# Optimization experiments

Measured on AMD Instinct MI355X. Metric: run time of the kernel, lower is better.

Reference implementation:

```python
import jax, jax.numpy as jnp
import numpy as np

N, E, D = 50000, 800000, 128
NODE_IN, EDGE_IN, STEPS = 19, 4, 5
EPS = 1e-5

def leaky(x):
    return jnp.where(x > 0, x, 0.05 * x)

def mlp3(x, W1, b1, W2, b2, W3, b3):
    x = leaky(x @ W1 + b1)
    x = leaky(x @ W2 + b2)
    return x @ W3 + b3

def layer_norm(x, g, b):
    m = jnp.mean(x, axis=-1, keepdims=True)
    v = jnp.var(x, axis=-1, keepdims=True)
    return (x - m) * jax.lax.rsqrt(v + EPS) * g + b

def batch_norm(x, g, b):
    # training-mode BatchNorm1d: biased batch stats over node dim
    m = jnp.mean(x, axis=0)
    v = jnp.var(x, axis=0)
    return (x - m) * jax.lax.rsqrt(v + EPS) * g + b

def gcn_conv(x, src, dst, W, b):
    # PyG GCNConv: add self loops, sym-normalize by deg^{-1/2}, aggregate at dst
    h = x @ W  # [N, D]
    deg = jax.ops.segment_sum(jnp.ones(E, x.dtype), dst, num_segments=N) + 1.0
    dis = jax.lax.rsqrt(deg)
    msg = h[src] * (dis[src] * dis[dst])[:, None]  # [E, D]
    agg = jax.ops.segment_sum(msg, dst, num_segments=N) + h * (dis * dis)[:, None]
    return agg + b


def setup_inputs() -> dict:
    key = jax.random.key(0)
    ks = iter(jax.random.split(key, 64))
    w = lambda shape: jax.random.normal(next(ks), shape, jnp.float32) * 0.05
    z = lambda: jnp.zeros((D,), jnp.float32)
    o = lambda: jnp.ones((D,), jnp.float32)
    inp = {
        'node_feat': jax.random.normal(next(ks), (N, NODE_IN), jnp.float32),
        'edge_feat': jax.random.normal(next(ks), (E, EDGE_IN), jnp.float32),
        'edge_index': jax.random.randint(next(ks), (2, E), 0, N, jnp.int32),
        'enc_node_W1': w((NODE_IN, D)), 'enc_node_b1': z(),
        'enc_node_W2': w((D, D)), 'enc_node_b2': z(),
        'enc_node_W3': w((D, D)), 'enc_node_b3': z(),
        'enc_node_ln_g': o(), 'enc_node_ln_b': z(),
        'enc_edge_W1': w((EDGE_IN, D)), 'enc_edge_b1': z(),
        'enc_edge_W2': w((D, D)), 'enc_edge_b2': z(),
        'enc_edge_W3': w((D, D)), 'enc_edge_b3': z(),
        'enc_edge_ln_g': o(), 'enc_edge_ln_b': z(),
        'proc_W': w((STEPS, 2, D, D)),
        'proc_b': jnp.zeros((STEPS, 2, D), jnp.float32),
        'proc_bn_g': jnp.ones((STEPS, D), jnp.float32),
        'proc_bn_b': jnp.zeros((STEPS, D), jnp.float32),
        'dec_W1': w((D, D)), 'dec_b1': z(),
        'dec_W2': w((D, D)), 'dec_b2': z(),
        'dec_W3': w((D, D)), 'dec_b3': z(),
        'dec_ln_g': o(), 'dec_ln_b': z(),
    }
    return inp


def reference(node_feat, edge_feat, edge_index,
              enc_node_W1, enc_node_b1, enc_node_W2, enc_node_b2, enc_node_W3, enc_node_b3,
              enc_node_ln_g, enc_node_ln_b,
              enc_edge_W1, enc_edge_b1, enc_edge_W2, enc_edge_b2, enc_edge_W3, enc_edge_b3,
              enc_edge_ln_g, enc_edge_ln_b,
              proc_W, proc_b, proc_bn_g, proc_bn_b,
              dec_W1, dec_b1, dec_W2, dec_b2, dec_W3, dec_b3, dec_ln_g, dec_ln_b):
    src, dst = edge_index[0], edge_index[1]
    # encode
    hn = layer_norm(mlp3(node_feat, enc_node_W1, enc_node_b1, enc_node_W2, enc_node_b2,
                         enc_node_W3, enc_node_b3), enc_node_ln_g, enc_node_ln_b)
    he = layer_norm(mlp3(edge_feat, enc_edge_W1, enc_edge_b1, enc_edge_W2, enc_edge_b2,
                         enc_edge_W3, enc_edge_b3), enc_edge_ln_g, enc_edge_ln_b)
    # scatter-mean edge features onto source nodes
    cnt = jax.ops.segment_sum(jnp.ones(E, hn.dtype), src, num_segments=N)
    hn = hn + jax.ops.segment_sum(he, src, num_segments=N) / jnp.maximum(cnt, 1.0)[:, None]
    # 5 residual GCN processor steps (GCNConv -> LeakyReLU -> BN -> GCNConv)
    for s in range(STEPS):
        x = gcn_conv(hn, src, dst, proc_W[s, 0], proc_b[s, 0])
        x = batch_norm(leaky(x), proc_bn_g[s], proc_bn_b[s])
        x = gcn_conv(x, src, dst, proc_W[s, 1], proc_b[s, 1])
        hn = hn + x
    # decode
    return layer_norm(mlp3(hn, dec_W1, dec_b1, dec_W2, dec_b2, dec_W3, dec_b3),
                      dec_ln_g, dec_ln_b)
```

## Files before the change

### kernel.cpp

```cpp
#include <hip/hip_runtime.h>

#define NN 50000
#define NE 800000
#define DD 128
#define LN_EPS 1e-5f

typedef __attribute__((ext_vector_type(8))) short v8s;
typedef __attribute__((ext_vector_type(4))) unsigned v4u;
typedef __attribute__((ext_vector_type(4))) float f32x4;
typedef __attribute__((ext_vector_type(2))) float f32x2;

union CvtHL { v4u u; v8s s; };

__device__ __forceinline__ float leakyf(float x){ return x > 0.f ? x : 0.05f*x; }
__device__ __forceinline__ short f2bf(float f){
  unsigned u = __float_as_uint(f);
  u = (u + 0x7fffu + ((u >> 16) & 1u)) >> 16;
  return (short)u;
}
__device__ __forceinline__ float bf2f(unsigned short h){
  return __uint_as_float(((unsigned)h) << 16);
}
__device__ __forceinline__ unsigned cvt_pk_bf16(float a, float b){
  unsigned r;
  asm("v_cvt_pk_bf16_f32 %0, %1, %2" : "=v"(r) : "v"(a), "v"(b));
  return r;
}
__device__ __forceinline__ f32x2 pk_add(f32x2 a, f32x2 b){
  f32x2 r; asm("v_pk_add_f32 %0, %1, %2" : "=v"(r) : "v"(a), "v"(b)); return r;
}
__device__ __forceinline__ f32x2 pk_mul(f32x2 a, f32x2 b){
  f32x2 r; asm("v_pk_mul_f32 %0, %1, %2" : "=v"(r) : "v"(a), "v"(b)); return r;
}
__device__ __forceinline__ unsigned pack_hi16(unsigned u0, unsigned u1){
  return __builtin_amdgcn_perm(u1, u0, 0x07060302u);
}
__device__ __forceinline__ short2 f2bf2v(float v){
  unsigned u = __float_as_uint(v);
  short hi = (short)(u >> 16);
  float lo = v - __uint_as_float(u & 0xffff0000u);
  return make_short2(hi, f2bf(lo));
}

__global__ void pack_w_kernel(const float* __restrict__ W, short* __restrict__ Wh,
                              short* __restrict__ Wl, int K, int Kp)
{
  int idx = blockIdx.x*256 + threadIdx.x;
  if (idx >= Kp*128) return;
  int k = idx >> 7, n = idx & 127;
  float v = (k < K) ? W[k*128 + n] : 0.f;
  short2 t = f2bf2v(v);
  size_t o = ((size_t)(k >> 3)*128 + n)*8 + (k & 7);
  Wh[o] = t.x; Wl[o] = t.y;
}

__global__ void pack_edge_w1_kernel(const float* __restrict__ W1, const float* __restrict__ b1,
                                    short* __restrict__ Wp)
{
  int idx = blockIdx.x*256 + threadIdx.x;
  if (idx >= 32*128) return;
  int k = idx >> 7, n = idx & 127;
  short v = 0;
  if (k < 4)        v = f2bf2v(W1[k*128 + n]).x;
  else if (k < 8)   v = f2bf2v(W1[(k-4)*128 + n]).y;
  else if (k < 12)  v = f2bf2v(W1[(k-8)*128 + n]).x;
  else if (k == 12) v = f2bf2v(b1[n]).x;
  else if (k == 13) v = f2bf2v(b1[n]).y;
  size_t o = ((size_t)(k >> 3)*128 + n)*8 + (k & 7);
  Wp[o] = v;
}

#define NPACK 11
struct PackArgs { const float* src[NPACK]; short* dh[NPACK]; short* dl[NPACK]; };

__global__ void pack_many_kernel(PackArgs pa)
{
  int m = blockIdx.y;
  int idx = blockIdx.x*256 + threadIdx.x;
  int k = idx >> 7, n = idx & 127;
  float v = pa.src[m][k*128 + n];
  short2 t = f2bf2v(v);
  size_t o = ((size_t)(k >> 3)*128 + n)*8 + (k & 7);
  pa.dh[m][o] = t.x; pa.dl[m][o] = t.y;
}

#define MFMA3(ah, al, bh, bl, ac) \
  ac = __builtin_amdgcn_mfma_f32_16x16x32_bf16(al, bh, ac, 0,0,0); \
  ac = __builtin_amdgcn_mfma_f32_16x16x32_bf16(ah, bl, ac, 0,0,0); \
  ac = __builtin_amdgcn_mfma_f32_16x16x32_bf16(ah, bh, ac, 0,0,0);

#define MFMA2(ah, bh, bl, ac) \
  ac = __builtin_amdgcn_mfma_f32_16x16x32_bf16(ah, bl, ac, 0,0,0); \
  ac = __builtin_amdgcn_mfma_f32_16x16x32_bf16(ah, bh, ac, 0,0,0);

#define SPLIT8(f0, f1, h, l) { \
  unsigned u0=__float_as_uint(f0.x), u1=__float_as_uint(f0.y), u2=__float_as_uint(f0.z), u3=__float_as_uint(f0.w); \
  unsigned u4=__float_as_uint(f1.x), u5=__float_as_uint(f1.y), u6=__float_as_uint(f1.z), u7=__float_as_uint(f1.w); \
  CvtHL ch_, cl_; \
  ch_.u = (v4u){ pack_hi16(u0,u1), pack_hi16(u2,u3), pack_hi16(u4,u5), pack_hi16(u6,u7) }; \
  cl_.u = (v4u){ \
    cvt_pk_bf16(f0.x-__uint_as_float(u0&0xffff0000u), f0.y-__uint_as_float(u1&0xffff0000u)), \
    cvt_pk_bf16(f0.z-__uint_as_float(u2&0xffff0000u), f0.w-__uint_as_float(u3&0xffff0000u)), \
    cvt_pk_bf16(f1.x-__uint_as_float(u4&0xffff0000u), f1.y-__uint_as_float(u5&0xffff0000u)), \
    cvt_pk_bf16(f1.z-__uint_as_float(u6&0xffff0000u), f1.w-__uint_as_float(u7&0xffff0000u)) }; \
  h = ch_.s; l = cl_.s; }

#define EPI_PK(accv, bv2, DOBIAS, p01, p23) { \
  f32x2 x01 = (f32x2){(accv)[0], (accv)[1]}; \
  f32x2 x23 = (f32x2){(accv)[2], (accv)[3]}; \
  if (DOBIAS) { x01 = pk_add(x01, bv2); x23 = pk_add(x23, bv2); } \
  f32x2 m01 = pk_mul(x01, (f32x2)(0.05f)); \
  f32x2 m23 = pk_mul(x23, (f32x2)(0.05f)); \
  p01 = cvt_pk_bf16(fmaxf(x01.x, m01.x), fmaxf(x01.y, m01.y)); \
  p23 = cvt_pk_bf16(fmaxf(x23.x, m23.x), fmaxf(x23.y, m23.y)); }

template<int IN_W, bool SCATTER>
__global__ __launch_bounds__(256)
void mlp_mfma_kernel(const float* __restrict__ x, int nrows,
                     const short* __restrict__ W1h, const short* __restrict__ W1l,
                     const float* __restrict__ b1,
                     const short* __restrict__ W2h, const short* __restrict__ W2l,
                     const float* __restrict__ b2,
                     const short* __restrict__ W3h, const short* __restrict__ W3l,
                     const float* __restrict__ b3,
                     const float* __restrict__ g, const float* __restrict__ bb,
                     float* __restrict__ out,
                     const int* __restrict__ sidx,
                     const int* __restrict__ eperm)
{
  constexpr int L1K = (IN_W + 31) / 32;
  constexpr bool EDGE1 = (SCATTER && IN_W == 4);
  __shared__ __align__(16) short Hh[128*136];
  __shared__ float lnS[128][2], lnQ[128][2];
  __shared__ int sidx_s[128];
  __shared__ __align__(16) uint4 xstage[SCATTER ? 128 : 1];

  const int tid  = threadIdx.x;
  const int lane = tid & 63, wave = tid >> 6;
  const int wr = wave >> 1, wc = wave & 1;
  const int quad = lane >> 4, low = lane & 15;
  const int row0 = blockIdx.x * 128;

  if (SCATTER) {
    if (tid < 128) {
      int e = eperm[row0 + tid];
      float4 f = ((const float4*)x)[e];
      unsigned u0=__float_as_uint(f.x), u1=__float_as_uint(f.y);
      unsigned u2=__float_as_uint(f.z), u3=__float_as_uint(f.w);
      uint4 st;
      st.x = pack_hi16(u0,u1);
      st.y = pack_hi16(u2,u3);
      st.z = cvt_pk_bf16(f.x-__uint_as_float(u0&0xffff0000u), f.y-__uint_as_float(u1&0xffff0000u));
      st.w = cvt_pk_bf16(f.z-__uint_as_float(u2&0xffff0000u), f.w-__uint_as_float(u3&0xffff0000u));
      xstage[tid] = st;
      sidx_s[tid] = sidx[row0 + tid];
    }
    __syncthreads();
  }

  f32x4 acc[4][4];

  #pragma unroll
  for (int tm=0;tm<4;tm++)
    #pragma unroll
    for (int tn=0;tn<4;tn++) acc[tm][tn] = (f32x4)0.f;

  if constexpr (EDGE1) {
    v8s ah[4], bh[4];
    #pragma unroll
    for (int tm=0;tm<4;tm++) {
      int lr = wr*64 + tm*16 + low;
      v8s h = (v8s)0;
      if (quad == 0) {
        uint4 st = xstage[lr];
        CvtHL c_; c_.u = (v4u){ st.x, st.y, st.x, st.y };
        h = c_.s;
      } else if (quad == 1) {
        uint4 st = xstage[lr];
        CvtHL c_; c_.u = (v4u){ st.z, st.w, 0x3F803F80u, 0u };
        h = c_.s;
      }
      ah[tm] = h;
    }
    #pragma unroll
    for (int tn=0;tn<4;tn++) {
      size_t o = ((size_t)quad*128 + wc*64 + tn*16 + low)*8;
      bh[tn] = *(const v8s*)(W1h + o);
    }
    #pragma unroll
    for (int tm=0;tm<4;tm++)
      #pragma unroll
      for (int tn=0;tn<4;tn++)
        acc[tm][tn] = __builtin_amdgcn_mfma_f32_16x16x32_bf16(ah[tm], bh[tn], acc[tm][tn], 0,0,0);
  } else {
    for (int ks = 0; ks < L1K; ks++) {
      v8s ah[4], al[4], bh[4], bl[4];
      #pragma unroll
      for (int tm=0;tm<4;tm++) {
        int lr = wr*64 + tm*16 + low;
        v8s h = (v8s)0, l = (v8s)0;
        if (IN_W % 32 == 0) {
          int r = row0 + lr;
          if (r < nrows) {
            const float* p = x + (size_t)r*IN_W + ks*32 + quad*8;
            float4 f0 = *(const float4*)p;
            float4 f1 = *(const float4*)(p + 4);
            SPLIT8(f0, f1, h, l);
          }
        } else {
          int r = row0 + lr;
          #pragma unroll
          for (int j=0;j<8;j++) {
            int k = ks*32 + quad*8 + j;
            if (k < IN_W && r < nrows) {
              short2 t = f2bf2v(x[(size_t)r*IN_W + k]);
              h[j] = t.x; l[j] = t.y;
            }
          }
        }
        ah[tm] = h; al[tm] = l;
      }
      #pragma unroll
      for (int tn=0;tn<4;tn++) {
        size_t o = ((size_t)(ks*4+quad)*128 + wc*64 + tn*16 + low)*8;
        bh[tn] = *(const v8s*)(W1h + o);
        bl[tn] = *(const v8s*)(W1l + o);
      }
      #pragma unroll
      for (int tm=0;tm<4;tm++)
        #pragma unroll
        for (int tn=0;tn<4;tn++) { MFMA3(ah[tm], al[tm], bh[tn], bl[tn], acc[tm][tn]); }
    }
  }
  #pragma unroll
  for (int tn=0;tn<4;tn++) {
    float bv = EDGE1 ? 0.f : b1[wc*64 + tn*16 + low];
    f32x2 bv2 = (f32x2)(bv);
    #pragma unroll
    for (int tm=0;tm<4;tm++) {
      unsigned p01, p23;
      EPI_PK(acc[tm][tn], bv2, !EDGE1, p01, p23);
      int base = (wr*64+tm*16+quad*4)*136 + wc*64+tn*16+low;
      Hh[base]     = (short)p01;
      Hh[base+136] = (short)(p01>>16);
      Hh[base+272] = (short)p23;
      Hh[base+408] = (short)(p23>>16);
    }
  }
  __syncthreads();

  #pragma unroll
  for (int tm=0;tm<4;tm++)
    #pragma unroll
    for (int tn=0;tn<4;tn++) acc[tm][tn] = (f32x4)0.f;
  #pragma unroll
  for (int ks=0;ks<4;ks++) {
    v8s ah[4], bh[4], bl[4];
    #pragma unroll
    for (int tm=0;tm<4;tm++)
      ah[tm] = *(const v8s*)&Hh[(wr*64+tm*16+low)*136 + ks*32 + quad*8];
    #pragma unroll
    for (int tn=0;tn<4;tn++) {
      size_t o = ((size_t)(ks*4+quad)*128 + wc*64 + tn*16 + low)*8;
      bh[tn] = *(const v8s*)(W2h + o);
      bl[tn] = *(const v8s*)(W2l + o);
    }
    #pragma unroll
    for (int tm=0;tm<4;tm++)
      #pragma unroll
      for (int tn=0;tn<4;tn++) { MFMA2(ah[tm], bh[tn], bl[tn], acc[tm][tn]); }
  }
  __syncthreads();
  #pragma unroll
  for (int tn=0;tn<4;tn++) {
    float bv = b2[wc*64 + tn*16 + low];
    f32x2 bv2 = (f32x2)(bv);
    #pragma unroll
    for (int tm=0;tm<4;tm++) {
      unsigned p01, p23;
      EPI_PK(acc[tm][tn], bv2, true, p01, p23);
      int base = (wr*64+tm*16+quad*4)*136 + wc*64+tn*16+low;
      Hh[base]     = (short)p01;
      Hh[base+136] = (short)(p01>>16);
      Hh[base+272] = (short)p23;
      Hh[base+408] = (short)(p23>>16);
    }
  }
  __syncthreads();

  #pragma unroll
  for (int tm=0;tm<4;tm++)
    #pragma unroll
    for (int tn=0;tn<4;tn++) acc[tm][tn] = (f32x4)0.f;
  #pragma unroll
  for (int ks=0;ks<4;ks++) {
    v8s ah[4], bh[4], bl[4];
    #pragma unroll
    for (int tm=0;tm<4;tm++)
      ah[tm] = *(const v8s*)&Hh[(wr*64+tm*16+low)*136 + ks*32 + quad*8];
    #pragma unroll
    for (int tn=0;tn<4;tn++) {
      size_t o = ((size_t)(ks*4+quad)*128 + wc*64 + tn*16 + low)*8;
      bh[tn] = *(const v8s*)(W3h + o);
      bl[tn] = *(const v8s*)(W3l + o);
    }
    #pragma unroll
    for (int tm=0;tm<4;tm++)
      #pragma unroll
      for (int tn=0;tn<4;tn++) { MFMA2(ah[tm], bh[tn], bl[tn], acc[tm][tn]); }
  }
  #pragma unroll
  for (int tn=0;tn<4;tn++) {
    float bv = b3[wc*64 + tn*16 + low];
    #pragma unroll
    for (int tm=0;tm<4;tm++)
      #pragma unroll
      for (int i=0;i<4;i++) acc[tm][tn][i] += bv;
  }

  {
    float ct[16];
    #pragma unroll
    for (int tm=0;tm<4;tm++)
      #pragma unroll
      for (int i=0;i<4;i++)
        ct[tm*4+i] = acc[tm][0][i] + acc[tm][1][i] + acc[tm][2][i] + acc[tm][3][i];
    #pragma unroll
    for (int st=0; st<4; st++) {
      const int mm = 1 << st;
      const bool hbit = ((low >> st) & 1) != 0;
      #pragma unroll
      for (int p=0; p < (16>>st); p+=2) {
        float snd = hbit ? ct[p]   : ct[p+1];
        float kp  = hbit ? ct[p+1] : ct[p];
        ct[p>>1] = kp + __shfl_xor(snd, mm);
      }
    }
    { int r = wr*64 + (low>>2)*16 + quad*4 + (low&3); lnS[r][wc] = ct[0]; }
    #pragma unroll
    for (int tm=0;tm<4;tm++)
      #pragma unroll
      for (int i=0;i<4;i++)
        ct[tm*4+i] = acc[tm][0][i]*acc[tm][0][i] + acc[tm][1][i]*acc[tm][1][i]
                   + acc[tm][2][i]*acc[tm][2][i] + acc[tm][3][i]*acc[tm][3][i];
    #pragma unroll
    for (int st=0; st<4; st++) {
      const int mm = 1 << st;
      const bool hbit = ((low >> st) & 1) != 0;
      #pragma unroll
      for (int p=0; p < (16>>st); p+=2) {
        float snd = hbit ? ct[p]   : ct[p+1];
        float kp  = hbit ? ct[p+1] : ct[p];
        ct[p>>1] = kp + __shfl_xor(snd, mm);
      }
    }
    { int r = wr*64 + (low>>2)*16 + quad*4 + (low&3); lnQ[r][wc] = ct[0]; }
  }
  __syncthreads();

  float g4[4], bb4[4];
  #pragma unroll
  for (int tn=0;tn<4;tn++) { int c = wc*64+tn*16+low; g4[tn] = g[c]; bb4[tn] = bb[c]; }

  #pragma unroll
  for (int tm=0;tm<4;tm++)
    #pragma unroll
    for (int i=0;i<4;i++) {
      int r = wr*64 + tm*16 + quad*4 + i;
      float2 S2 = *(const float2*)&lnS[r][0];
      float2 Q2 = *(const float2*)&lnQ[r][0];
      float s = S2.x + S2.y;
      float q = Q2.x + Q2.y;
      float m = s * (1.f/128.f);
      float var = q * (1.f/128.f) - m*m;
      float rs = rsqrtf(var + LN_EPS);
      int gr = row0 + r;
      if (!SCATTER && gr >= nrows) continue;
      float v0 = (acc[tm][0][i] - m) * rs * g4[0] + bb4[0];
      float v1 = (acc[tm][1][i] - m) * rs * g4[1] + bb4[1];
      float v2 = (acc[tm][2][i] - m) * rs * g4[2] + bb4[2];
      float v3 = (acc[tm][3][i] - m) * rs * g4[3] + bb4[3];
      if (SCATTER) {
        unsigned p01 = cvt_pk_bf16(v0, v1), p23 = cvt_pk_bf16(v2, v3);
        int base = r*132 + wc*64 + low;
        Hh[base]    = (short)p01;
        Hh[base+16] = (short)(p01>>16);
        Hh[base+32] = (short)p23;
        Hh[base+48] = (short)(p23>>16);
      } else {
        size_t ob = (size_t)gr*DD + wc*64 + low;
        out[ob]    = v0;
        out[ob+16] = v1;
        out[ob+32] = v2;
        out[ob+48] = v3;
      }
    }

  if (SCATTER) {
    __syncthreads();
    const unsigned* H32 = (const unsigned*)Hh;
    int cp = tid & 63;
    int gI = tid >> 6;
    int rbeg = gI*32, rend = rbeg + 32;
    unsigned pv = H32[rbeg*66 + cp];
    float a0 = __uint_as_float(pv << 16), a1 = __uint_as_float(pv & 0xffff0000u);
    int cur = sidx_s[rbeg];
    for (int r = rbeg + 1; r < rend; r++) {
      int sv = sidx_s[r];
      unsigned hv = H32[r*66 + cp];
      if (sv != cur) {
        atomicAdd(&out[(size_t)cur*DD + 2*cp],     a0);
        atomicAdd(&out[(size_t)cur*DD + 2*cp + 1], a1);
        a0 = __uint_as_float(hv << 16); a1 = __uint_as_float(hv & 0xffff0000u);
        cur = sv;
      } else {
        a0 += __uint_as_float(hv << 16); a1 += __uint_as_float(hv & 0xffff0000u);
      }
    }
    atomicAdd(&out[(size_t)cur*DD + 2*cp],     a0);
    atomicAdd(&out[(size_t)cur*DD + 2*cp + 1], a1);
  }
}

__global__ __launch_bounds__(256)
void gemm_mfma_kernel(const float* __restrict__ x,
                      const short* __restrict__ Wh, const short* __restrict__ Wl,
                      const float* __restrict__ initv, const float* __restrict__ rowscale,
                      unsigned short* __restrict__ outbf, int nrows)
{
  const int tid  = threadIdx.x;
  const int lane = tid & 63, wave = tid >> 6;
  const int wr = wave >> 1, wc = wave & 1;
  const int quad = lane >> 4, low = lane & 15;
  const int row0 = blockIdx.x * 64;

  f32x4 acc[2][4];
  #pragma unroll
  for (int tm=0;tm<2;tm++)
    #pragma unroll
    for (int tn=0;tn<4;tn++) acc[tm][tn] = (f32x4)0.f;

  #pragma unroll
  for (int ks=0;ks<4;ks++) {
    v8s ah[2], al[2], bh[4], bl[4];
    #pragma unroll
    for (int tm=0;tm<2;tm++) {
      int r = row0 + wr*32 + tm*16 + low;
      v8s h = (v8s)0, l = (v8s)0;
      if (r < nrows) {
        const float* p = x + (size_t)r*DD + ks*32 + quad*8;
        float4 f0 = *(const float4*)p;
        float4 f1 = *(const float4*)(p + 4);
        SPLIT8(f0, f1, h, l);
      }
      ah[tm] = h; al[tm] = l;
    }
    #pragma unroll
    for (int tn=0;tn<4;tn++) {
      size_t o = ((size_t)(ks*4+quad)*128 + wc*64 + tn*16 + low)*8;
      bh[tn] = *(const v8s*)(Wh + o);
      bl[tn] = *(const v8s*)(Wl + o);
    }
    #pragma unroll
    for (int tm=0;tm<2;tm++)
      #pragma unroll
      for (int tn=0;tn<4;tn++) { MFMA3(ah[tm], al[tm], bh[tn], bl[tn], acc[tm][tn]); }
  }

  float iv4[4];
  #pragma unroll
  for (int tn=0;tn<4;tn++) iv4[tn] = initv ? initv[wc*64 + tn*16 + low] : 0.f;

  #pragma unroll
  for (int tm=0;tm<2;tm++)
    #pragma unroll
    for (int i=0;i<4;i++) {
      int gr = row0 + wr*32 + tm*16 + quad*4 + i;
      if (gr >= nrows) continue;
      float sc = rowscale ? rowscale[gr] : 1.f;
      float v0 = (acc[tm][0][i] + iv4[0]) * sc;
      float v1 = (acc[tm][1][i] + iv4[1]) * sc;
      float v2 = (acc[tm][2][i] + iv4[2]) * sc;
      float v3 = (acc[tm][3][i] + iv4[3]) * sc;
      unsigned p01 = cvt_pk_bf16(v0, v1), p23 = cvt_pk_bf16(v2, v3);
      size_t base = (size_t)gr*DD + wc*64 + low;
      outbf[base]    = (unsigned short)p01;
      outbf[base+16] = (unsigned short)(p01>>16);
      outbf[base+32] = (unsigned short)p23;
      outbf[base+48] = (unsigned short)(p23>>16);
    }
}

__global__ __launch_bounds__(256)
void gemm_bf_mfma_kernel(const unsigned short* __restrict__ xb,
                         const short* __restrict__ Wh, const short* __restrict__ Wl,
                         const float* __restrict__ initv, const float* __restrict__ rowscale,
                         unsigned short* __restrict__ outbf, int nrows)
{
  const int tid  = threadIdx.x;
  const int lane = tid & 63, wave = tid >> 6;
  const int wr = wave >> 1, wc = wave & 1;
  const int quad = lane >> 4, low = lane & 15;
  const int row0 = blockIdx.x * 64;

  f32x4 acc[2][4];
  #pragma unroll
  for (int tm=0;tm<2;tm++)
    #pragma unroll
    for (int tn=0;tn<4;tn++) acc[tm][tn] = (f32x4)0.f;

  #pragma unroll
  for (int ks=0;ks<4;ks++) {
    v8s ah[2], bh[4], bl[4];
    #pragma unroll
    for (int tm=0;tm<2;tm++) {
      int r = row0 + wr*32 + tm*16 + low;
      ah[tm] = (r < nrows) ? *(const v8s*)(xb + (size_t)r*DD + ks*32 + quad*8) : (v8s)0;
    }
    #pragma unroll
    for (int tn=0;tn<4;tn++) {
      size_t o = ((size_t)(ks*4+quad)*128 + wc*64 + tn*16 + low)*8;
      bh[tn] = *(const v8s*)(Wh + o);
      bl[tn] = *(const v8s*)(Wl + o);
    }
    #pragma unroll
    for (int tm=0;tm<2;tm++)
      #pragma unroll
      for (int tn=0;tn<4;tn++) { MFMA2(ah[tm], bh[tn], bl[tn], acc[tm][tn]); }
  }

  float iv4[4];
  #pragma unroll
  for (int tn=0;tn<4;tn++) iv4[tn] = initv ? initv[wc*64 + tn*16 + low] : 0.f;

  #pragma unroll
  for (int tm=0;tm<2;tm++)
    #pragma unroll
    for (int i=0;i<4;i++) {
      int gr = row0 + wr*32 + tm*16 + quad*4 + i;
      if (gr >= nrows) continue;
      float sc = rowscale ? rowscale[gr] : 1.f;
      float v0 = (acc[tm][0][i] + iv4[0]) * sc;
      float v1 = (acc[tm][1][i] + iv4[1]) * sc;
      float v2 = (acc[tm][2][i] + iv4[2]) * sc;
      float v3 = (acc[tm][3][i] + iv4[3]) * sc;
      unsigned p01 = cvt_pk_bf16(v0, v1), p23 = cvt_pk_bf16(v2, v3);
      size_t base = (size_t)gr*DD + wc*64 + low;
      outbf[base]    = (unsigned short)p01;
      outbf[base+16] = (unsigned short)(p01>>16);
      outbf[base+32] = (unsigned short)p23;
      outbf[base+48] = (unsigned short)(p23>>16);
    }
}

#define ADD8(a, vv) { \
  a[0] += __uint_as_float((vv).x << 16); a[1] += __uint_as_float((vv).x & 0xffff0000u); \
  a[2] += __uint_as_float((vv).y << 16); a[3] += __uint_as_float((vv).y & 0xffff0000u); \
  a[4] += __uint_as_float((vv).z << 16); a[5] += __uint_as_float((vv).z & 0xffff0000u); \
  a[6] += __uint_as_float((vv).w << 16); a[7] += __uint_as_float((vv).w & 0xffff0000u); }

__global__ __launch_bounds__(256)
void gcn_agg_kernel(const unsigned* __restrict__ hb, const int* __restrict__ rowptr,
                    const int* __restrict__ csr_src, const float* __restrict__ dis,
                    const float* __restrict__ bias, const float* __restrict__ resid,
                    float* __restrict__ outf, unsigned* __restrict__ outb, int mode)
{
  const int wv = __builtin_amdgcn_readfirstlane(threadIdx.x >> 6);
  const int lane = threadIdx.x & 63;
  const int q4 = lane >> 4;
  const int c4 = lane & 15;
  const uint4* hb4 = (const uint4*)hb;
  for (int i = blockIdx.x*4 + wv; i < NN; i += gridDim.x*4) {
    const int beg = rowptr[i], end = rowptr[i+1];
    float a[8];
    #pragma unroll
    for (int t=0;t<8;t++) a[t] = 0.f;
    if (q4 == 0) {
      uint4 sv = hb4[(size_t)i*16 + c4];
      ADD8(a, sv);
    }
    int j = beg;
    for (; j + 16 <= end; j += 16) {
      uint4 v[4];
      #pragma unroll
      for (int k=0;k<4;k++) {
        int s0=csr_src[j+4*k], s1=csr_src[j+4*k+1], s2=csr_src[j+4*k+2], s3=csr_src[j+4*k+3];
        int s = q4==0 ? s0 : q4==1 ? s1 : q4==2 ? s2 : s3;
        v[k] = hb4[(size_t)s*16 + c4];
      }
      #pragma unroll
      for (int k=0;k<4;k++) ADD8(a, v[k]);
    }
    for (; j + 4 <= end; j += 4) {
      int s0=csr_src[j], s1=csr_src[j+1], s2=csr_src[j+2], s3=csr_src[j+3];
      int s = q4==0 ? s0 : q4==1 ? s1 : q4==2 ? s2 : s3;
      uint4 v = hb4[(size_t)s*16 + c4];
      ADD8(a, v);
    }
    if (j < end) {
      int rem = end - j;
      int s = csr_src[j + (q4 < rem ? q4 : 0)];
      uint4 v = hb4[(size_t)s*16 + c4];
      if (q4 < rem) ADD8(a, v);
    }
    #pragma unroll
    for (int t=0;t<8;t++) { a[t] += __shfl_xor(a[t], 16); a[t] += __shfl_xor(a[t], 32); }
    float di = dis[i];
    float4 b0 = ((const float4*)bias)[2*c4], b1 = ((const float4*)bias)[2*c4+1];
    a[0]=a[0]*di+b0.x; a[1]=a[1]*di+b0.y; a[2]=a[2]*di+b0.z; a[3]=a[3]*di+b0.w;
    a[4]=a[4]*di+b1.x; a[5]=a[5]*di+b1.y; a[6]=a[6]*di+b1.z; a[7]=a[7]*di+b1.w;
    if (mode == 0) {
      if (q4 == 0) {
        uint4 pk;
        pk.x = cvt_pk_bf16(leakyf(a[0]), leakyf(a[1]));
        pk.y = cvt_pk_bf16(leakyf(a[2]), leakyf(a[3]));
        pk.z = cvt_pk_bf16(leakyf(a[4]), leakyf(a[5]));
        pk.w = cvt_pk_bf16(leakyf(a[6]), leakyf(a[7]));
        ((uint4*)outb)[(size_t)i*16 + c4] = pk;
      }
    } else {
      if (q4 == 0) {
        float4 r0 = ((const float4*)resid)[(size_t)i*32 + 2*c4];
        float4 r1 = ((const float4*)resid)[(size_t)i*32 + 2*c4+1];
        r0.x+=a[0]; r0.y+=a[1]; r0.z+=a[2]; r0.w+=a[3];
        r1.x+=a[4]; r1.y+=a[5]; r1.z+=a[6]; r1.w+=a[7];
        ((float4*)outf)[(size_t)i*32 + 2*c4]   = r0;
        ((float4*)outf)[(size_t)i*32 + 2*c4+1] = r1;
      }
    }
  }
}

__global__ void count_kernel(const int* __restrict__ src, const int* __restrict__ dst,
                             int* __restrict__ cnt_src, int* __restrict__ deg_dst)
{
  int e = blockIdx.x*blockDim.x + threadIdx.x;
  if (e < NE) {
    atomicAdd(&cnt_src[src[e]], 1);
    atomicAdd(&deg_dst[dst[e]], 1);
  }
}

__global__ void scan2_kernel(const int* __restrict__ a0, int* __restrict__ r0, int* __restrict__ n0,
                             float* __restrict__ aux0,
                             const int* __restrict__ a1, int* __restrict__ r1, int* __restrict__ n1,
                             float* __restrict__ aux1)
{
  const int* a = blockIdx.x ? a1 : a0;
  int* r = blockIdx.x ? r1 : r0;
  int* n = blockIdx.x ? n1 : n0;
  float* aux = blockIdx.x ? aux1 : aux0;
  const int T = 256;
  int tid = threadIdx.x;
  int chunk = (NN + T - 1) / T;
  int begin = tid*chunk, end = begin + chunk; if (end > NN) end = NN; if (begin > NN) begin = NN;
  int s = 0;
  for (int i = begin; i < end; i++) s += a[i];
  __shared__ int ps[T];
  ps[tid] = s; __syncthreads();
  for (int off = 1; off < T; off <<= 1) {
    int v = 0;
    if (tid >= off) v = ps[tid - off];
    __syncthreads();
    if (tid >= off) ps[tid] += v;
    __syncthreads();
  }
  int base = (tid == 0) ? 0 : ps[tid-1];
  for (int i = begin; i < end; i++) {
    r[i] = base; n[i] = base; base += a[i];
    aux[i] = blockIdx.x ? (1.0f / fmaxf((float)a[i], 1.0f)) : rsqrtf((float)a[i] + 1.0f);
  }
  if (tid == T-1) r[NN] = base;
}

__global__ void fill_both_kernel(const int* __restrict__ src, const int* __restrict__ dst,
                                 int* __restrict__ nextp, int* __restrict__ csr_src,
                                 int* __restrict__ nexts, int* __restrict__ eperm,
                                 int* __restrict__ srcsorted)
{
  int e = blockIdx.x*blockDim.x + threadIdx.x;
  if (e < NE) {
    int s = src[e];
    int pos = atomicAdd(&nextp[dst[e]], 1);
    csr_src[pos] = s;
    int ps = atomicAdd(&nexts[s], 1);
    eperm[ps] = e;
    srcsorted[ps] = s;
  }
}

__global__ void addmean_kernel(float* __restrict__ hn, const float* __restrict__ nodesum,
                               const float* __restrict__ invcnt)
{
  int t = blockIdx.x*blockDim.x + threadIdx.x;
  if (t < NN*DD/4) {
    float4 a = ((const float4*)hn)[t];
    float4 b = ((const float4*)nodesum)[t];
    float ic = invcnt[t >> 5];
    a.x += b.x*ic; a.y += b.y*ic; a.z += b.z*ic; a.w += b.w*ic;
    ((float4*)hn)[t] = a;
  }
}

__global__ __launch_bounds__(256)
void bn_stats_kernel(const unsigned short* __restrict__ yb, float* __restrict__ sums)
{
  int col = threadIdx.x & 127, grp = threadIdx.x >> 7;
  float s = 0.f, ss = 0.f;
  for (int i = blockIdx.x*2 + grp; i < NN; i += gridDim.x*2) {
    float v = bf2f(yb[(size_t)i*DD + col]);
    s += v; ss += v*v;
  }
  __shared__ float ls[256], lss[256];
  ls[threadIdx.x] = s; lss[threadIdx.x] = ss;
  __syncthreads();
  if (grp == 0) {
    atomicAdd(&sums[col],      ls[col]  + ls[col+128]);
    atomicAdd(&sums[DD + col], lss[col] + lss[col+128]);
  }
}

__global__ __launch_bounds__(256)
void bn_fold_kernel(const float* __restrict__ sums, const float* __restrict__ g,
                    const float* __restrict__ b, const float* __restrict__ W2,
                    short* __restrict__ Wfh, short* __restrict__ Wfl,
                    float* __restrict__ cvec)
{
  __shared__ float scale_s[DD], shift_s[DD];
  int tid = threadIdx.x;
  if (tid < DD) {
    float m = sums[tid] / (float)NN;
    float var = sums[DD + tid] / (float)NN - m*m;
    float is = rsqrtf(var + LN_EPS);
    float sc = is * g[tid];
    scale_s[tid] = sc;
    shift_s[tid] = b[tid] - m * sc;
  }
  __syncthreads();
  int col = tid & 127, kh = tid >> 7;
  float cpart = 0.f;
  #pragma unroll
  for (int kk = 0; kk < 4; kk++) {
    int k = blockIdx.x*8 + kh*4 + kk;
    float w = W2[k*DD + col];
    short2 t = f2bf2v(w * scale_s[k]);
    size_t o = ((size_t)(k >> 3)*128 + col)*8 + (k & 7);
    Wfh[o] = t.x; Wfl[o] = t.y;
    cpart += shift_s[k] * w;
  }
  atomicAdd(&cvec[col], cpart);
}

extern "C" void kernel_launch(void* const* d_in, const int* in_sizes, int n_in,
                              void* d_out, int out_size, void* d_ws, size_t ws_size,
                              hipStream_t stream)
{
  const float* node_feat = (const float*)d_in[0];
  const float* edge_feat = (const float*)d_in[1];
  const int*   edge_index = (const int*)d_in[2];
  const int* src = edge_index;
  const int* dst = edge_index + NE;

  const float* enW1 = (const float*)d_in[3];  const float* enb1 = (const float*)d_in[4];
  const float* enW2 = (const float*)d_in[5];  const float* enb2 = (const float*)d_in[6];
  const float* enW3 = (const float*)d_in[7];  const float* enb3 = (const float*)d_in[8];
  const float* enlg = (const float*)d_in[9];  const float* enlb = (const float*)d_in[10];

  const float* eeW1 = (const float*)d_in[11]; const float* eeb1 = (const float*)d_in[12];
  const float* eeW2 = (const float*)d_in[13]; const float* eeb2 = (const float*)d_in[14];
  const float* eeW3 = (const float*)d_in[15]; const float* eeb3 = (const float*)d_in[16];
  const float* eelg = (const float*)d_in[17]; const float* eelb = (const float*)d_in[18];

  const float* procW = (const float*)d_in[19];
  const float* procB = (const float*)d_in[20];
  const float* bnG   = (const float*)d_in[21];
  const float* bnB   = (const float*)d_in[22];

  const float* dW1 = (const float*)d_in[23]; const float* db1 = (const float*)d_in[24];
  const float* dW2 = (const float*)d_in[25]; const float* db2 = (const float*)d_in[26];
  const float* dW3 = (const float*)d_in[27]; const float* db3 = (const float*)d_in[28];
  const float* dlg = (const float*)d_in[29]; const float* dlb = (const float*)d_in[30];

  char* ws = (char*)d_ws;
  size_t off = 0;
  auto alloc = [&](size_t bytes) -> void* {
    void* p = ws + off;
    off = (off + bytes + 255) & ~(size_t)255;
    return p;
  };
  float* hn     = (float*)alloc((size_t)NN*DD*4);
  float* esum   = (float*)alloc((size_t)NN*DD*4);
  unsigned short* hbf = (unsigned short*)alloc((size_t)NN*DD*2);
  unsigned short* ybf = (unsigned short*)alloc((size_t)NN*DD*2);
  float* dis    = (float*)alloc(NN*4);
  float* invcnt = (float*)alloc(NN*4);
  float* bnsums = (float*)alloc(3*DD*4);
  float* cvec   = bnsums + 2*DD;
  int* deg    = (int*)alloc(NN*4);
  int* cnt    = (int*)alloc(NN*4);
  int* rowptr = (int*)alloc((NN+1)*4);
  int* nextp  = (int*)alloc(NN*4);
  int* srow   = (int*)alloc((NN+1)*4);
  int* nexts  = (int*)alloc(NN*4);
  int* csr    = (int*)alloc((size_t)NE*4);
  int* eperm  = (int*)alloc((size_t)NE*4);
  int* srcsorted = (int*)alloc((size_t)NE*4);
  auto allocW = [&](int kp) { return (short*)alloc((size_t)kp*128*2); };
  short *pN1h=allocW(32),  *pN1l=allocW(32);
  short *pN2h=allocW(128), *pN2l=allocW(128);
  short *pN3h=allocW(128), *pN3l=allocW(128);
  short *pE1h=allocW(32),  *pE1l=allocW(32);
  short *pE2h=allocW(128), *pE2l=allocW(128);
  short *pE3h=allocW(128), *pE3l=allocW(128);
  short *pD1h=allocW(128), *pD1l=allocW(128);
  short *pD2h=allocW(128), *pD2l=allocW(128);
  short *pD3h=allocW(128), *pD3l=allocW(128);
  short *pP0h[5], *pP0l[5];
  for (int s = 0; s < 5; s++) { pP0h[s]=allocW(128); pP0l[s]=allocW(128); }
  short *pWfh=allocW(128), *pWfl=allocW(128);

  (void)hipMemsetAsync(deg, 0, NN*4, stream);
  (void)hipMemsetAsync(cnt, 0, NN*4, stream);
  (void)hipMemsetAsync(esum, 0, (size_t)NN*DD*4, stream);

  PackArgs pa;
  const float* s128[NPACK] = { enW2, enW3, eeW2, eeW3, dW1, dW2, dW3,
                               procW + 0*(size_t)DD*DD*2, procW + 1*(size_t)DD*DD*2,
                               procW + 2*(size_t)DD*DD*2, procW + 3*(size_t)DD*DD*2 };
  short* d128h[NPACK] = { pN2h, pN3h, pE2h, pE3h, pD1h, pD2h, pD3h, pP0h[0], pP0h[1], pP0h[2], pP0h[3] };
  short* d128l[NPACK] = { pN2l, pN3l, pE2l, pE3l, pD1l, pD2l, pD3l, pP0l[0], pP0l[1], pP0l[2], pP0l[3] };
  for (int m = 0; m < NPACK; m++) { pa.src[m]=s128[m]; pa.dh[m]=d128h[m]; pa.dl[m]=d128l[m]; }
  pack_many_kernel<<<dim3(64, NPACK), 256, 0, stream>>>(pa);
  const int G32 = (32*128+255)/256, G128 = (128*128+255)/256;
  pack_w_kernel<<<G32, 256, 0, stream>>>(enW1, pN1h, pN1l, 19, 32);
  pack_edge_w1_kernel<<<G32, 256, 0, stream>>>(eeW1, eeb1, pE1h);
  pack_w_kernel<<<G128,256, 0, stream>>>(procW + 4*(size_t)DD*DD*2, pP0h[4], pP0l[4], 128, 128);

  count_kernel<<<(NE+255)/256, 256, 0, stream>>>(src, dst, cnt, deg);
  scan2_kernel<<<2, 256, 0, stream>>>(deg, rowptr, nextp, dis, cnt, srow, nexts, invcnt);
  fill_both_kernel<<<(NE+255)/256, 256, 0, stream>>>(src, dst, nextp, csr, nexts, eperm, srcsorted);

  const int GN  = (NN + 127) / 128;
  const int GE  = NE / 128;
  const int GG  = (NN + 63) / 64;
  const int GA  = 2048;

  mlp_mfma_kernel<19, false><<<GN, 256, 0, stream>>>(node_feat, NN,
      pN1h, pN1l, enb1, pN2h, pN2l, enb2, pN3h, pN3l, enb3, enlg, enlb, hn,
      nullptr, nullptr);
  mlp_mfma_kernel<4, true><<<GE, 256, 0, stream>>>(edge_feat, NE,
      pE1h, pE1l, eeb1, pE2h, pE2l, eeb2, pE3h, pE3l, eeb3, eelg, eelb, esum,
      srcsorted, eperm);
  addmean_kernel<<<(NN*DD/4+255)/256, 256, 0, stream>>>(hn, esum, invcnt);

  for (int s = 0; s < 5; s++) {
    const float* Wc2 = procW + (size_t)(s*2+1)*DD*DD;
    const float* b0  = procB + (size_t)(s*2+0)*DD;
    const float* b1p = procB + (size_t)(s*2+1)*DD;

    gemm_mfma_kernel<<<GG, 256, 0, stream>>>(hn, pP0h[s], pP0l[s], nullptr, dis, hbf, NN);
    gcn_agg_kernel<<<GA, 256, 0, stream>>>((const unsigned*)hbf, rowptr, csr, dis,
                                           b0, nullptr, nullptr, (unsigned*)ybf, 0);
    (void)hipMemsetAsync(bnsums, 0, 3*DD*4, stream);
    bn_stats_kernel<<<512, 256, 0, stream>>>(ybf, bnsums);
    bn_fold_kernel<<<16, 256, 0, stream>>>(bnsums, bnG + s*DD, bnB + s*DD, Wc2, pWfh, pWfl, cvec);
    gemm_bf_mfma_kernel<<<GG, 256, 0, stream>>>(ybf, pWfh, pWfl, cvec, dis, hbf, NN);
    gcn_agg_kernel<<<GA, 256, 0, stream>>>((const unsigned*)hbf, rowptr, csr, dis,
                                           b1p, hn, hn, nullptr, 1);
  }

  mlp_mfma_kernel<128, false><<<GN, 256, 0, stream>>>(hn, NN,
      pD1h, pD1l, db1, pD2h, pD2l, db2, pD3h, pD3l, db3, dlg, dlb, (float*)d_out,
      nullptr, nullptr);
}
```

Measured before the change: 1.364 ms.

## Remap GCN aggregation to one wave per node with 4-byte lane loads

The gather-aggregate kernel now gives each wave a whole node row, with each lane holding two bf16 columns (4 bytes), instead of splitting edges across four 16-lane groups with 16-byte loads and a cross-lane shuffle reduction. The grid becomes one wave per node rather than a grid-stride loop, which removes the shuffle reduction and the idle lanes in the epilogue. The cost is narrower loads, 256 bytes per edge per wave instead of 64 bytes per lane group, plus more serial edge iterations per wave. Separately, the batch-norm stats kernel reads packed bf16 pairs as 32-bit words and reduces four row groups per block.

```diff
diff --git a/kernel.cpp b/kernel.cpp
--- a/kernel.cpp
+++ b/kernel.cpp
@@ -553,12 +553,6 @@
     }
 }
 
-#define ADD8(a, vv) { \
-  a[0] += __uint_as_float((vv).x << 16); a[1] += __uint_as_float((vv).x & 0xffff0000u); \
-  a[2] += __uint_as_float((vv).y << 16); a[3] += __uint_as_float((vv).y & 0xffff0000u); \
-  a[4] += __uint_as_float((vv).z << 16); a[5] += __uint_as_float((vv).z & 0xffff0000u); \
-  a[6] += __uint_as_float((vv).w << 16); a[7] += __uint_as_float((vv).w & 0xffff0000u); }
-
 __global__ __launch_bounds__(256)
 void gcn_agg_kernel(const unsigned* __restrict__ hb, const int* __restrict__ rowptr,
                     const int* __restrict__ csr_src, const float* __restrict__ dis,
@@ -567,67 +561,46 @@
 {
   const int wv = __builtin_amdgcn_readfirstlane(threadIdx.x >> 6);
   const int lane = threadIdx.x & 63;
-  const int q4 = lane >> 4;
-  const int c4 = lane & 15;
-  const uint4* hb4 = (const uint4*)hb;
-  for (int i = blockIdx.x*4 + wv; i < NN; i += gridDim.x*4) {
-    const int beg = rowptr[i], end = rowptr[i+1];
-    float a[8];
-    #pragma unroll
-    for (int t=0;t<8;t++) a[t] = 0.f;
-    if (q4 == 0) {
-      uint4 sv = hb4[(size_t)i*16 + c4];
-      ADD8(a, sv);
-    }
-    int j = beg;
-    for (; j + 16 <= end; j += 16) {
-      uint4 v[4];
-      #pragma unroll
-      for (int k=0;k<4;k++) {
-        int s0=csr_src[j+4*k], s1=csr_src[j+4*k+1], s2=csr_src[j+4*k+2], s3=csr_src[j+4*k+3];
-        int s = q4==0 ? s0 : q4==1 ? s1 : q4==2 ? s2 : s3;
-        v[k] = hb4[(size_t)s*16 + c4];
-      }
-      #pragma unroll
-      for (int k=0;k<4;k++) ADD8(a, v[k]);
-    }
-    for (; j + 4 <= end; j += 4) {
-      int s0=csr_src[j], s1=csr_src[j+1], s2=csr_src[j+2], s3=csr_src[j+3];
-      int s = q4==0 ? s0 : q4==1 ? s1 : q4==2 ? s2 : s3;
-      uint4 v = hb4[(size_t)s*16 + c4];
-      ADD8(a, v);
-    }
-    if (j < end) {
-      int rem = end - j;
-      int s = csr_src[j + (q4 < rem ? q4 : 0)];
-      uint4 v = hb4[(size_t)s*16 + c4];
-      if (q4 < rem) ADD8(a, v);
-    }
-    #pragma unroll
-    for (int t=0;t<8;t++) { a[t] += __shfl_xor(a[t], 16); a[t] += __shfl_xor(a[t], 32); }
-    float di = dis[i];
-    float4 b0 = ((const float4*)bias)[2*c4], b1 = ((const float4*)bias)[2*c4+1];
-    a[0]=a[0]*di+b0.x; a[1]=a[1]*di+b0.y; a[2]=a[2]*di+b0.z; a[3]=a[3]*di+b0.w;
-    a[4]=a[4]*di+b1.x; a[5]=a[5]*di+b1.y; a[6]=a[6]*di+b1.z; a[7]=a[7]*di+b1.w;
-    if (mode == 0) {
-      if (q4 == 0) {
-        uint4 pk;
-        pk.x = cvt_pk_bf16(leakyf(a[0]), leakyf(a[1]));
-        pk.y = cvt_pk_bf16(leakyf(a[2]), leakyf(a[3]));
-        pk.z = cvt_pk_bf16(leakyf(a[4]), leakyf(a[5]));
-        pk.w = cvt_pk_bf16(leakyf(a[6]), leakyf(a[7]));
-        ((uint4*)outb)[(size_t)i*16 + c4] = pk;
-      }
-    } else {
-      if (q4 == 0) {
-        float4 r0 = ((const float4*)resid)[(size_t)i*32 + 2*c4];
-        float4 r1 = ((const float4*)resid)[(size_t)i*32 + 2*c4+1];
-        r0.x+=a[0]; r0.y+=a[1]; r0.z+=a[2]; r0.w+=a[3];
-        r1.x+=a[4]; r1.y+=a[5]; r1.z+=a[6]; r1.w+=a[7];
-        ((float4*)outf)[(size_t)i*32 + 2*c4]   = r0;
-        ((float4*)outf)[(size_t)i*32 + 2*c4+1] = r1;
-      }
-    }
+  const int i = blockIdx.x*4 + wv;
+  if (i >= NN) return;
+  unsigned hv = hb[(size_t)i*64 + lane];
+  float ax = bf2f((unsigned short)(hv & 0xffff)), ay = bf2f((unsigned short)(hv >> 16));
+  const int beg = rowptr[i], end = rowptr[i+1];
+  int j = beg;
+  for (; j + 16 <= end; j += 16) {
+    unsigned v[16];
+    #pragma unroll
+    for (int k=0;k<16;k++) v[k] = hb[(size_t)csr_src[j+k]*64 + lane];
+    #pragma unroll
+    for (int k=0;k<16;k++) {
+      ax += bf2f((unsigned short)(v[k] & 0xffff));
+      ay += bf2f((unsigned short)(v[k] >> 16));
+    }
+  }
+  for (; j + 4 <= end; j += 4) {
+    unsigned v[4];
+    #pragma unroll
+    for (int k=0;k<4;k++) v[k] = hb[(size_t)csr_src[j+k]*64 + lane];
+    #pragma unroll
+    for (int k=0;k<4;k++) {
+      ax += bf2f((unsigned short)(v[k] & 0xffff));
+      ay += bf2f((unsigned short)(v[k] >> 16));
+    }
+  }
+  for (; j < end; j++) {
+    unsigned v = hb[(size_t)csr_src[j]*64 + lane];
+    ax += bf2f((unsigned short)(v & 0xffff));
+    ay += bf2f((unsigned short)(v >> 16));
+  }
+  float di = dis[i];
+  ax = ax*di + bias[2*lane]; ay = ay*di + bias[2*lane+1];
+  size_t o = (size_t)i*64 + lane;
+  if (mode == 0) {
+    outb[o] = cvt_pk_bf16(leakyf(ax), leakyf(ay));
+  } else {
+    float2 rs = ((const float2*)resid)[o];
+    float2 r; r.x = rs.x + ax; r.y = rs.y + ay;
+    ((float2*)outf)[o] = r;
   }
 }
 
@@ -703,20 +676,30 @@
 }
 
 __global__ __launch_bounds__(256)
-void bn_stats_kernel(const unsigned short* __restrict__ yb, float* __restrict__ sums)
-{
-  int col = threadIdx.x & 127, grp = threadIdx.x >> 7;
-  float s = 0.f, ss = 0.f;
-  for (int i = blockIdx.x*2 + grp; i < NN; i += gridDim.x*2) {
-    float v = bf2f(yb[(size_t)i*DD + col]);
-    s += v; ss += v*v;
-  }
-  __shared__ float ls[256], lss[256];
-  ls[threadIdx.x] = s; lss[threadIdx.x] = ss;
+void bn_stats_kernel(const unsigned* __restrict__ yb32, float* __restrict__ sums)
+{
+  int cp  = threadIdx.x & 63;
+  int grp = threadIdx.x >> 6;
+  float s0=0.f, s1=0.f, q0=0.f, q1=0.f;
+  for (int i = blockIdx.x*4 + grp; i < NN; i += gridDim.x*4) {
+    unsigned v = yb32[(size_t)i*64 + cp];
+    float a = __uint_as_float(v << 16);
+    float b = __uint_as_float(v & 0xffff0000u);
+    s0 += a; q0 += a*a; s1 += b; q1 += b*b;
+  }
+  __shared__ float red[256][4];
+  red[threadIdx.x][0]=s0; red[threadIdx.x][1]=s1; red[threadIdx.x][2]=q0; red[threadIdx.x][3]=q1;
   __syncthreads();
   if (grp == 0) {
-    atomicAdd(&sums[col],      ls[col]  + ls[col+128]);
-    atomicAdd(&sums[DD + col], lss[col] + lss[col+128]);
+    float t0=0.f,t1=0.f,t2=0.f,t3=0.f;
+    #pragma unroll
+    for (int g2=0; g2<4; g2++) {
+      t0+=red[g2*64+cp][0]; t1+=red[g2*64+cp][1]; t2+=red[g2*64+cp][2]; t3+=red[g2*64+cp][3];
+    }
+    atomicAdd(&sums[2*cp],      t0);
+    atomicAdd(&sums[2*cp+1],    t1);
+    atomicAdd(&sums[DD+2*cp],   t2);
+    atomicAdd(&sums[DD+2*cp+1], t3);
   }
 }
 
@@ -843,7 +826,7 @@
   const int GN  = (NN + 127) / 128;
   const int GE  = NE / 128;
   const int GG  = (NN + 63) / 64;
-  const int GA  = 2048;
+  const int GA  = (NN + 3) / 4;
 
   mlp_mfma_kernel<19, false><<<GN, 256, 0, stream>>>(node_feat, NN,
       pN1h, pN1l, enb1, pN2h, pN2l, enb2, pN3h, pN3l, enb3, enlg, enlb, hn,
@@ -862,7 +845,7 @@
     gcn_agg_kernel<<<GA, 256, 0, stream>>>((const unsigned*)hbf, rowptr, csr, dis,
                                            b0, nullptr, nullptr, (unsigned*)ybf, 0);
     (void)hipMemsetAsync(bnsums, 0, 3*DD*4, stream);
-    bn_stats_kernel<<<512, 256, 0, stream>>>(ybf, bnsums);
+    bn_stats_kernel<<<512, 256, 0, stream>>>((const unsigned*)ybf, bnsums);
     bn_fold_kernel<<<16, 256, 0, stream>>>(bnsums, bnG + s*DD, bnB + s*DD, Wc2, pWfh, pWfl, cvec);
     gemm_bf_mfma_kernel<<<GG, 256, 0, stream>>>(ybf, pWfh, pWfl, cvec, dis, hbf, NN);
     gcn_agg_kernel<<<GA, 256, 0, stream>>>((const unsigned*)hbf, rowptr, csr, dis,
```

Result: no change. 1.374 ms (+0.7%).
